# Kernel tuning notes

Hardware: AMD Instinct MI355X
Metric: run time of the kernel (lower is better)

Reference implementation:

```python
import jax, jax.numpy as jnp
import numpy as np


def _bilinear_sample(x, gx, gy):
    # x: (N,C,H,W); gx,gy: (L,H,W) normalized coords in [-1,1]
    # Matches torch.nn.functional.grid_sample(mode='bilinear',
    # padding_mode='zeros', align_corners=True).
    N, C, H, W = x.shape
    ix = (gx + 1.0) * 0.5 * (W - 1)  # unnormalize to pixel coords
    iy = (gy + 1.0) * 0.5 * (H - 1)
    ix0 = jnp.floor(ix)
    iy0 = jnp.floor(iy)
    wx1 = ix - ix0
    wy1 = iy - iy0
    wx0 = 1.0 - wx1
    wy0 = 1.0 - wy1

    def g(iy_, ix_, w):
        valid = (ix_ >= 0) & (ix_ <= W - 1) & (iy_ >= 0) & (iy_ <= H - 1)
        ic = jnp.clip(ix_, 0, W - 1).astype(jnp.int32)
        jc = jnp.clip(iy_, 0, H - 1).astype(jnp.int32)
        v = x[:, :, jc, ic]  # (N,C,L,H,W) gather
        return v * (w * valid.astype(x.dtype))

    return (g(iy0, ix0, wy0 * wx0)
            + g(iy0, ix0 + 1.0, wy0 * wx1)
            + g(iy0 + 1.0, ix0, wy1 * wx0)
            + g(iy0 + 1.0, ix0 + 1.0, wy1 * wx1))


def _radon(x, theta):
    # x: (N,C,W,W), theta: (L,) angles in degrees
    N, C, H, W = x.shape
    rad = theta.astype(x.dtype) * (jnp.pi / 180.0)
    c, s = jnp.cos(rad), jnp.sin(rad)
    base = jnp.linspace(-1.0, 1.0, W, dtype=x.dtype)  # align_corners=True grid
    X = base[None, None, :]   # (1,1,W) varies along width
    Y = base[None, :, None]   # (1,W,1) varies along height
    # affine_grid with R = [[c, s, 0], [-s, c, 0]]
    gx = c[:, None, None] * X + s[:, None, None] * Y   # (L,W,W)
    gy = -s[:, None, None] * X + c[:, None, None] * Y  # (L,W,W)
    samp = _bilinear_sample(x, gx, gy)                 # (N,C,L,W,W)
    out = samp.sum(axis=3)                             # line integral over rows -> (N,C,L,W)
    return jnp.swapaxes(out, -1, -2)                   # (N,C,W,L) sinogram


def setup_inputs() -> dict:
    key = jax.random.key(0)
    x = jax.random.normal(key, (2, 1, 512, 512), dtype=jnp.float32)
    theta = jnp.arange(180, dtype=jnp.float32)
    return {"x": x, "theta": theta}


def reference(x, theta):
    return _radon(x, theta)
```

## Files before the change

### kernel.cpp

```cpp
#include <hip/hip_runtime.h>

#define IMG   512
#define WT    64
#define HT    64
#define NSTRIP (IMG / HT)
#define NT    512
#define HC    8
#define HPER  (HT / HC)
#define ROWS  96
#define PITCH_A 95
#define PITCH_B 97
#define TILE_FLOATS (ROWS * PITCH_B + 8)

__device__ __forceinline__ void gload_lds4(const float* g, float* l) {
    __builtin_amdgcn_global_load_lds((const __attribute__((address_space(1))) void*)g,
                                     (__attribute__((address_space(3))) void*)l,
                                     4, 0, 0);
}

__device__ __forceinline__ float vfract(float x) {
    float r;
    asm("v_fract_f32 %0, %1" : "=v"(r) : "v"(x));
    return r;
}

template<int PITCH>
__device__ __forceinline__ float lerp4(const float* __restrict__ tile,
                                       float fx, float fy) {
    int jx = (int)fx;
    int jy = (int)fy;
    const float* __restrict__ p = tile + (__mul24(jy, PITCH) + jx);
    float v00 = p[0];
    float v01 = p[1];
    float v10 = p[PITCH];
    float v11 = p[PITCH + 1];
    float wx1 = vfract(fx);
    float wy1 = vfract(fy);
    float lx0 = fmaf(wx1, v01 - v00, v00);
    float lx1 = fmaf(wx1, v11 - v10, v10);
    return fmaf(wy1, lx1 - lx0, lx0);
}

template<int PITCH>
__device__ __forceinline__ void radon_body(
    const float* __restrict__ img, float* __restrict__ tile,
    float* __restrict__ out, float s, float c,
    int n, int a, int w0, int A)
{
    int lane = threadIdx.x & 63;
    int wv   = threadIdx.x >> 6;

    float u   = (float)(w0 + lane) - 255.5f;
    float uc  = (float)w0 + (31.5f - 255.5f);
    float ex  = (fabsf(c) + s) * 31.5f;
    float ixc = fmaf(c, uc, fmaf(s, (31.5f - 255.5f), 255.5f));
    float iyc = fmaf(-s, uc, fmaf(c, (31.5f - 255.5f), 255.5f));

    float acc = 0.0f;
    for (int st = 0; st < NSTRIP; ++st) {
        int xmin = (int)floorf(ixc - ex) - 1;
        int ymin = (int)floorf(iyc - ex) - 1;
        int dx   = (int)floorf(ixc + ex) - (xmin + 1);
        int dy   = (int)floorf(iyc + ex) - (ymin + 1);
        int nxn  = min(dx + 4, PITCH);
        int nyn  = min(dy + 4, ROWS);

        if (st > 0) __syncthreads();

        bool border = (xmin < 0) | (ymin < 0) | (xmin + nxn > IMG) | (ymin + nyn > IMG);
        if (!border) {
            for (int yy = wv; yy < nyn; yy += HC) {
                const float* __restrict__ src = img + (size_t)(ymin + yy) * IMG + xmin;
                float* dst = tile + __mul24(yy, PITCH);
                gload_lds4(src + lane, dst);
                if (64 + lane < nxn) gload_lds4(src + 64 + lane, dst + 64);
            }
        } else {
            int total4 = (__mul24(nyn, PITCH) + 3) >> 2;
            float4 z = make_float4(0.f, 0.f, 0.f, 0.f);
            for (int i = threadIdx.x; i < total4; i += NT)
                ((float4*)tile)[i] = z;
            __syncthreads();
            int gx0 = max(xmin, 0), gx1 = min(xmin + nxn, IMG);
            int gy0 = max(ymin, 0), gy1 = min(ymin + nyn, IMG);
            int lx0 = gx0 - xmin;
            for (int gy = gy0 + wv; gy < gy1; gy += HC) {
                int yy = gy - ymin;
                const float* __restrict__ src = img + (size_t)gy * IMG;
                float* dst = tile + (__mul24(yy, PITCH) + lx0);
                for (int k = 0; gx0 + k < gx1; k += 64)
                    if (gx0 + k + lane < gx1)
                        gload_lds4(src + gx0 + k + lane, dst + k);
            }
        }
        __syncthreads();

        float tb = (float)(st * HT + wv * HPER) - 255.5f;
        float fx = fmaf(s, tb, fmaf(c,  u, 255.5f - (float)xmin));
        float fy = fmaf(c, tb, fmaf(-s, u, 255.5f - (float)ymin));
        #pragma unroll
        for (int b = 0; b < HPER / 4; ++b) {
            float fx0 = fx,       fy0 = fy;
            float fx1 = fx0 + s,  fy1 = fy0 + c;
            float fx2 = fx1 + s,  fy2 = fy1 + c;
            float fx3 = fx2 + s,  fy3 = fy2 + c;
            fx = fx3 + s;  fy = fy3 + c;
            acc += lerp4<PITCH>(tile, fx0, fy0);
            acc += lerp4<PITCH>(tile, fx1, fy1);
            acc += lerp4<PITCH>(tile, fx2, fy2);
            acc += lerp4<PITCH>(tile, fx3, fy3);
        }

        ixc += s * (float)HT;
        iyc += c * (float)HT;
    }

    __syncthreads();
    tile[threadIdx.x] = acc;
    __syncthreads();
    if (threadIdx.x < WT) {
        float r = 0.0f;
        #pragma unroll
        for (int k = 0; k < HC; ++k) r += tile[k * WT + threadIdx.x];
        out[((size_t)n * IMG + w0 + threadIdx.x) * A + a] = r;
    }
}

__global__ __launch_bounds__(NT, 8) void radon_lds(
    const float* __restrict__ x, const float* __restrict__ theta,
    float* __restrict__ out, int N, int A)
{
    __shared__ float tile[TILE_FLOATS];
    int a  = blockIdx.z % A;
    int n  = blockIdx.z / A;
    int w0 = blockIdx.x * WT;

    float rad = theta[a] * (3.14159265358979323846f / 180.0f);
    float s, c;
    __sincosf(rad, &s, &c);

    const float* __restrict__ img = x + (size_t)n * (IMG * IMG);
    if (c * s >= 0.0f)
        radon_body<PITCH_A>(img, tile, out, s, c, n, a, w0, A);
    else
        radon_body<PITCH_B>(img, tile, out, s, c, n, a, w0, A);
}

extern "C" void kernel_launch(void* const* d_in, const int* in_sizes, int n_in,
                              void* d_out, int out_size, void* d_ws, size_t ws_size,
                              hipStream_t stream) {
    const float* x     = (const float*)d_in[0];
    const float* theta = (const float*)d_in[1];
    float* out = (float*)d_out;

    int A = in_sizes[1];
    int N = in_sizes[0] / (IMG * IMG);

    dim3 grid(IMG / WT, 1, N * A);
    radon_lds<<<grid, NT, 0, stream>>>(x, theta, out, N, A);
}
```

Before: 91.58 us.

## Store LDS tile rows flipped for positive cosine to use single pitch

Replaces the two pitch-specialized template instantiations with one kernel that uses a single pitch of 97, and stores tile rows in reversed order when cos is non-negative. The sampling y coordinate and its step are mirrored to match, so LDS bank-conflict behaviour is handled by the row flip instead of by choosing between pitches. The border path now zeroes only the needed rows, using an lgkmcnt wait instead of a barrier before issuing async global-to-LDS loads. The reduction moves to a separate shared array. Code size shrinks, but every index computation now carries extra select logic.

```diff
diff --git a/kernel.cpp b/kernel.cpp
--- a/kernel.cpp
+++ b/kernel.cpp
@@ -1,21 +1,19 @@
 #include <hip/hip_runtime.h>
 
-#define IMG   512
-#define WT    64
-#define HT    64
+#define IMG    512
+#define WT     64
+#define HT     64
 #define NSTRIP (IMG / HT)
-#define NT    512
-#define HC    8
-#define HPER  (HT / HC)
-#define ROWS  96
-#define PITCH_A 95
-#define PITCH_B 97
-#define TILE_FLOATS (ROWS * PITCH_B + 8)
+#define NT     512
+#define HC     8
+#define HPER   (HT / HC)
+#define ROWS   96
+#define PITCH  97
+#define BUF_FLOATS (ROWS * PITCH + 8)
 
 __device__ __forceinline__ void gload_lds4(const float* g, float* l) {
     __builtin_amdgcn_global_load_lds((const __attribute__((address_space(1))) void*)g,
-                                     (__attribute__((address_space(3))) void*)l,
-                                     4, 0, 0);
+                                     (__attribute__((address_space(3))) void*)l, 4, 0, 0);
 }
 
 __device__ __forceinline__ float vfract(float x) {
@@ -24,7 +22,6 @@
     return r;
 }
 
-template<int PITCH>
 __device__ __forceinline__ float lerp4(const float* __restrict__ tile,
                                        float fx, float fy) {
     int jx = (int)fx;
@@ -41,12 +38,24 @@
     return fmaf(wy1, lx1 - lx0, lx0);
 }
 
-template<int PITCH>
-__device__ __forceinline__ void radon_body(
-    const float* __restrict__ img, float* __restrict__ tile,
-    float* __restrict__ out, float s, float c,
-    int n, int a, int w0, int A)
+__global__ __launch_bounds__(NT, 8) void radon_lds(
+    const float* __restrict__ x, const float* __restrict__ theta,
+    float* __restrict__ out, int N, int A)
 {
+    __shared__ float tile[BUF_FLOATS];
+    __shared__ float red[NT];
+    int a  = blockIdx.z % A;
+    int n  = blockIdx.z / A;
+    int w0 = blockIdx.x * WT;
+
+    float rad = theta[a] * 0.017453292519943295f;
+    float s, c;
+    __sincosf(rad, &s, &c);
+
+    bool  flip = (c >= 0.0f);
+    float cE   = flip ? -c : c;
+
+    const float* __restrict__ img = x + (size_t)n * (IMG * IMG);
     int lane = threadIdx.x & 63;
     int wv   = threadIdx.x >> 6;
 
@@ -60,10 +69,8 @@
     for (int st = 0; st < NSTRIP; ++st) {
         int xmin = (int)floorf(ixc - ex) - 1;
         int ymin = (int)floorf(iyc - ex) - 1;
-        int dx   = (int)floorf(ixc + ex) - (xmin + 1);
-        int dy   = (int)floorf(iyc + ex) - (ymin + 1);
-        int nxn  = min(dx + 4, PITCH);
-        int nyn  = min(dy + 4, ROWS);
+        int nxn  = min((int)floorf(ixc + ex) - xmin + 3, PITCH);
+        int nyn  = min((int)floorf(iyc + ex) - ymin + 3, ROWS);
 
         if (st > 0) __syncthreads();
 
@@ -71,44 +78,47 @@
         if (!border) {
             for (int yy = wv; yy < nyn; yy += HC) {
                 const float* __restrict__ src = img + (size_t)(ymin + yy) * IMG + xmin;
-                float* dst = tile + __mul24(yy, PITCH);
+                float* dst = tile + __mul24(flip ? (nyn - 1 - yy) : yy, PITCH);
                 gload_lds4(src + lane, dst);
                 if (64 + lane < nxn) gload_lds4(src + 64 + lane, dst + 64);
             }
         } else {
-            int total4 = (__mul24(nyn, PITCH) + 3) >> 2;
-            float4 z = make_float4(0.f, 0.f, 0.f, 0.f);
-            for (int i = threadIdx.x; i < total4; i += NT)
-                ((float4*)tile)[i] = z;
-            __syncthreads();
             int gx0 = max(xmin, 0), gx1 = min(xmin + nxn, IMG);
-            int gy0 = max(ymin, 0), gy1 = min(ymin + nyn, IMG);
-            int lx0 = gx0 - xmin;
-            for (int gy = gy0 + wv; gy < gy1; gy += HC) {
-                int yy = gy - ymin;
-                const float* __restrict__ src = img + (size_t)gy * IMG;
-                float* dst = tile + (__mul24(yy, PITCH) + lx0);
-                for (int k = 0; gx0 + k < gx1; k += 64)
-                    if (gx0 + k + lane < gx1)
-                        gload_lds4(src + gx0 + k + lane, dst + k);
+            int lx0 = gx0 - xmin, lxn = gx1 - gx0;
+            for (int yy = wv; yy < nyn; yy += HC) {
+                float* dst = tile + __mul24(flip ? (nyn - 1 - yy) : yy, PITCH);
+                for (int xx = lane; xx < nxn; xx += 64) dst[xx] = 0.0f;
+            }
+            asm volatile("s_waitcnt lgkmcnt(0)" ::: "memory");
+            if (lxn > 0) {
+                for (int yy = wv; yy < nyn; yy += HC) {
+                    int gy = ymin + yy;
+                    if ((unsigned)gy < (unsigned)IMG) {
+                        const float* __restrict__ src = img + (size_t)gy * IMG + gx0;
+                        float* dst = tile + (__mul24(flip ? (nyn - 1 - yy) : yy, PITCH) + lx0);
+                        for (int k = 0; k < lxn; k += 64)
+                            if (k + lane < lxn) gload_lds4(src + k + lane, dst + k);
+                    }
+                }
             }
         }
         __syncthreads();
 
-        float tb = (float)(st * HT + wv * HPER) - 255.5f;
-        float fx = fmaf(s, tb, fmaf(c,  u, 255.5f - (float)xmin));
-        float fy = fmaf(c, tb, fmaf(-s, u, 255.5f - (float)ymin));
+        float tb  = (float)(st * HT + wv * HPER) - 255.5f;
+        float fx  = fmaf(s, tb, fmaf(c,  u, 255.5f - (float)xmin));
+        float fyo = fmaf(c, tb, fmaf(-s, u, 255.5f - (float)ymin));
+        float fy  = flip ? ((float)(nyn - 1) - fyo) : fyo;
         #pragma unroll
         for (int b = 0; b < HPER / 4; ++b) {
-            float fx0 = fx,       fy0 = fy;
-            float fx1 = fx0 + s,  fy1 = fy0 + c;
-            float fx2 = fx1 + s,  fy2 = fy1 + c;
-            float fx3 = fx2 + s,  fy3 = fy2 + c;
-            fx = fx3 + s;  fy = fy3 + c;
-            acc += lerp4<PITCH>(tile, fx0, fy0);
-            acc += lerp4<PITCH>(tile, fx1, fy1);
-            acc += lerp4<PITCH>(tile, fx2, fy2);
-            acc += lerp4<PITCH>(tile, fx3, fy3);
+            float fx0 = fx,        fy0 = fy;
+            float fx1 = fx0 + s,   fy1 = fy0 + cE;
+            float fx2 = fx1 + s,   fy2 = fy1 + cE;
+            float fx3 = fx2 + s,   fy3 = fy2 + cE;
+            fx = fx3 + s;  fy = fy3 + cE;
+            acc += lerp4(tile, fx0, fy0);
+            acc += lerp4(tile, fx1, fy1);
+            acc += lerp4(tile, fx2, fy2);
+            acc += lerp4(tile, fx3, fy3);
         }
 
         ixc += s * (float)HT;
@@ -116,34 +126,14 @@
     }
 
     __syncthreads();
-    tile[threadIdx.x] = acc;
+    red[threadIdx.x] = acc;
     __syncthreads();
     if (threadIdx.x < WT) {
         float r = 0.0f;
         #pragma unroll
-        for (int k = 0; k < HC; ++k) r += tile[k * WT + threadIdx.x];
+        for (int k = 0; k < HC; ++k) r += red[k * WT + threadIdx.x];
         out[((size_t)n * IMG + w0 + threadIdx.x) * A + a] = r;
     }
-}
-
-__global__ __launch_bounds__(NT, 8) void radon_lds(
-    const float* __restrict__ x, const float* __restrict__ theta,
-    float* __restrict__ out, int N, int A)
-{
-    __shared__ float tile[TILE_FLOATS];
-    int a  = blockIdx.z % A;
-    int n  = blockIdx.z / A;
-    int w0 = blockIdx.x * WT;
-
-    float rad = theta[a] * (3.14159265358979323846f / 180.0f);
-    float s, c;
-    __sincosf(rad, &s, &c);
-
-    const float* __restrict__ img = x + (size_t)n * (IMG * IMG);
-    if (c * s >= 0.0f)
-        radon_body<PITCH_A>(img, tile, out, s, c, n, a, w0, A);
-    else
-        radon_body<PITCH_B>(img, tile, out, s, c, n, a, w0, A);
 }
 
 extern "C" void kernel_launch(void* const* d_in, const int* in_sizes, int n_in,
```

Measured after the change: 127.0 us. 1.39x slower.
